# Performance work log

Hardware: AMD Instinct MI355X
Metric: run time of the kernel (lower is better)

Reference implementation:

```python
import jax, jax.numpy as jnp
import numpy as np

HIDDEN = 1024
HEADS = 16
HEAD_DIM = HIDDEN // HEADS


def setup_inputs() -> dict:
    key = jax.random.key(0)
    ks = jax.random.split(key, 9)
    B, S = 2, 2048
    std = 1.0 / np.sqrt(HIDDEN)
    inp = {
        'hidden_states': jax.random.normal(ks[0], (B, S, HIDDEN), dtype=jnp.float32),
        'attention_mask': jnp.ones((B, S), dtype=jnp.int32),
        'wq': jax.random.normal(ks[1], (HIDDEN, HIDDEN), dtype=jnp.float32) * std,
        'bq': jnp.zeros((HIDDEN,), dtype=jnp.float32),
        'wk': jax.random.normal(ks[2], (HIDDEN, HIDDEN), dtype=jnp.float32) * std,
        'bk': jnp.zeros((HIDDEN,), dtype=jnp.float32),
        'wv': jax.random.normal(ks[3], (HIDDEN, HIDDEN), dtype=jnp.float32) * std,
        'bv': jnp.zeros((HIDDEN,), dtype=jnp.float32),
        'wo': jax.random.normal(ks[4], (HIDDEN, HIDDEN), dtype=jnp.float32) * std,
        'bo': jnp.zeros((HIDDEN,), dtype=jnp.float32),
    }
    return inp


def reference(hidden_states, attention_mask, wq, bq, wk, bk, wv, bv, wo, bo):
    B, S, H = hidden_states.shape
    def heads(x):  # [B,S,H] -> [B,nh,S,hd]
        return x.reshape(B, S, HEADS, HEAD_DIM).transpose(0, 2, 1, 3)
    q = heads(hidden_states @ wq + bq)
    k = heads(hidden_states @ wk + bk)
    v = heads(hidden_states @ wv + bv)
    scores = jnp.einsum('bhqd,bhkd->bhqk', q, k) / np.sqrt(HEAD_DIM).astype(np.float32)
    causal = jnp.tril(jnp.ones((S, S), dtype=bool))  # True = keep
    keep = causal[None, None] & (attention_mask[:, None, None, :] != 0)
    scores = jnp.where(keep, scores, -jnp.inf)
    probs = jax.nn.softmax(scores, axis=-1)
    out = jnp.einsum('bhqk,bhkd->bhqd', probs, v)  # [B,nh,S,hd]
    out = out.transpose(0, 2, 1, 3).reshape(B, S, H)
    return out @ wo + bo
```

## Files before the change

kernel.cpp:

```cpp
#include <hip/hip_runtime.h>

#define HID   1024
#define SLEN  2048
#define NHEAD 16
#define HDIM  64
#define SC2L  0.18033688f

typedef unsigned short u16;
typedef _Float16 f16;
using bf16x8 = __attribute__((ext_vector_type(8))) short;
using f16x4  = __attribute__((ext_vector_type(4))) f16;
using f32x4  = __attribute__((ext_vector_type(4))) float;

typedef __attribute__((address_space(1))) void gvoid;
typedef __attribute__((address_space(3))) void lvoid;

__device__ __forceinline__ u16 f2bf(float f) {
  union { float f; unsigned u; } v; v.f = f;
  unsigned u = v.u;
  return (u16)((u + 0x7fffu + ((u >> 16) & 1u)) >> 16);
}

__device__ __forceinline__ void async_ld16(const u16* g, u16* l) {
  __builtin_amdgcn_global_load_lds((gvoid*)g, (lvoid*)l, 16, 0, 0);
}

__global__ __launch_bounds__(256) void prep_kernel(const float* __restrict__ x,
                                                   const float* __restrict__ wq,
                                                   const float* __restrict__ wk,
                                                   const float* __restrict__ wv,
                                                   const float* __restrict__ wo,
                                                   u16* __restrict__ xb,
                                                   u16* __restrict__ wt) {
  const int tid = threadIdx.x;
  if (blockIdx.z == 4) {
    const int bid = blockIdx.y * 32 + blockIdx.x;
#pragma unroll
    for (int it = 0; it < 4; ++it) {
      const int i = bid * 1024 + it * 256 + tid;
      float4 v = ((const float4*)x)[i];
      ushort4 o;
      o.x = f2bf(v.x); o.y = f2bf(v.y); o.z = f2bf(v.z); o.w = f2bf(v.w);
      ((ushort4*)xb)[i] = o;
    }
    return;
  }
  const float* src = (blockIdx.z == 0) ? wq : (blockIdx.z == 1) ? wk
                   : (blockIdx.z == 2) ? wv : wo;
  u16* dst = wt + (size_t)blockIdx.z * (HID * HID);
  __shared__ float tile[32][33];
  const int n0 = blockIdx.x * 32, k0 = blockIdx.y * 32;
  const int xx = tid & 31, yy = tid >> 5;
  for (int i = yy; i < 32; i += 8)
    tile[i][xx] = src[(size_t)(k0 + i) * HID + n0 + xx];
  __syncthreads();
  for (int i = yy; i < 32; i += 8)
    dst[(size_t)(n0 + i) * HID + k0 + xx] = f2bf(tile[xx][i]);
}

__global__ __launch_bounds__(256) void gemm_qkv_kernel(const u16* __restrict__ A,
                                                       const u16* __restrict__ Bt,
                                                       const float* __restrict__ bq,
                                                       const float* __restrict__ bk,
                                                       const float* __restrict__ bv,
                                                       u16* __restrict__ Qb,
                                                       u16* __restrict__ Kb,
                                                       u16* __restrict__ VTf) {
  __shared__ u16 smem[8192];
  u16* sA = smem;
  u16* sB = smem + 4096;
  const int tid  = threadIdx.x;
  const int wave = tid >> 6, lane = tid & 63;
  const int quad = lane >> 4, l16 = lane & 15;
  const int n0g = blockIdx.x * 128;
  const int region = blockIdx.x >> 3;
  const int colbase = (blockIdx.x & 7) * 128;
  const int m0 = blockIdx.y * 128;
  const int wm = (wave & 1) * 64, wn = (wave >> 1) * 64;

  f32x4 acc[4][4] = {};
  const int srow = lane >> 2;
  const int scol = (lane & 3) * 8;

  for (int kt = 0; kt < HID; kt += 32) {
    __syncthreads();
    for (int c = wave; c < 8; c += 4) {
      async_ld16(A  + (size_t)(m0  + c * 16 + srow) * HID + kt + scol, &sA[c * 512]);
      async_ld16(Bt + (size_t)(n0g + c * 16 + srow) * HID + kt + scol, &sB[c * 512]);
    }
    __syncthreads();

    bf16x8 af[4], bfr[4];
#pragma unroll
    for (int t = 0; t < 4; ++t) {
      af[t]  = *(const bf16x8*)&sA[(wm + t * 16 + l16) * 32 + quad * 8];
      bfr[t] = *(const bf16x8*)&sB[(wn + t * 16 + l16) * 32 + quad * 8];
    }
#pragma unroll
    for (int mt = 0; mt < 4; ++mt)
#pragma unroll
      for (int nt = 0; nt < 4; ++nt)
        acc[mt][nt] = __builtin_amdgcn_mfma_f32_16x16x32_bf16(af[mt], bfr[nt],
                                                              acc[mt][nt], 0, 0, 0);
  }

  const float* bias = (region == 0) ? bq : (region == 1) ? bk : bv;
  float bvv[4];
#pragma unroll
  for (int nt = 0; nt < 4; ++nt) bvv[nt] = bias[colbase + wn + nt * 16 + l16];

  if (region == 2) {
    const int bb = m0 >> 11;
    const int m0loc = m0 & 2047;
    const int h0 = colbase >> 6;
    u16* T = smem;
#pragma unroll
    for (int h2 = 0; h2 < 2; ++h2) {
      __syncthreads();
      if ((wave >> 1) == h2) {
#pragma unroll
        for (int mt = 0; mt < 4; ++mt)
#pragma unroll
          for (int nt = 0; nt < 4; ++nt)
#pragma unroll
            for (int r = 0; r < 4; ++r) {
              const int sl = (wave & 1) * 64 + mt * 16 + quad * 4 + r;
              const int dl = nt * 16 + l16;
              union { f16 h; u16 u; } cv;
              cv.h = (f16)(acc[mt][nt][r] + bvv[nt]);
              T[dl * 128 + (((sl >> 3) ^ l16) * 8) + (sl & 7)] = cv.u;
            }
      }
      __syncthreads();
      const int d = tid >> 2, sg = (tid & 3) * 4;
      u16* slab0 = VTf + ((size_t)((bb * NHEAD + h0 + h2) * 128 + (m0loc >> 4))) * 1024;
#pragma unroll
      for (int cc = 0; cc < 4; ++cc) {
        const int cl = sg + cc;
        const int ph = cl ^ (d & 15);
        const int slot = (d * 2 + (cl & 1)) ^ ((d >> 2) & 1);
        *(bf16x8*)(slab0 + (size_t)(cl >> 1) * 1024 + slot * 8)
            = *(const bf16x8*)&T[d * 128 + ph * 8];
      }
    }
    return;
  }

  u16* C = (region == 0) ? Qb : Kb;
#pragma unroll
  for (int mt = 0; mt < 4; ++mt)
#pragma unroll
    for (int r = 0; r < 4; ++r) {
      const int row = m0 + wm + mt * 16 + quad * 4 + r;
#pragma unroll
      for (int nt = 0; nt < 4; ++nt) {
        const int col = colbase + wn + nt * 16 + l16;
        C[(size_t)row * HID + col] = f2bf(acc[mt][nt][r] + bvv[nt]);
      }
    }
}

__global__ __launch_bounds__(256) void gemm_o_kernel(const u16* __restrict__ A,
                                                     const u16* __restrict__ Bt,
                                                     const float* __restrict__ bias,
                                                     float* __restrict__ Cf) {
  __shared__ u16 sA[64 * 32];
  __shared__ u16 sB[128 * 32];
  const int tid  = threadIdx.x;
  const int wave = tid >> 6, lane = tid & 63;
  const int quad = lane >> 4, l16 = lane & 15;
  const int n0 = blockIdx.x * 128;
  const int m0 = blockIdx.y * 64;
  const int wn = wave * 32;

  f32x4 acc[4][2] = {};
  const int srow = lane >> 2;
  const int scol = (lane & 3) * 8;

  for (int kt = 0; kt < HID; kt += 32) {
    __syncthreads();
    for (int c = wave; c < 12; c += 4) {
      if (c < 4) async_ld16(A  + (size_t)(m0 + c * 16 + srow) * HID + kt + scol, &sA[c * 512]);
      else       async_ld16(Bt + (size_t)(n0 + (c - 4) * 16 + srow) * HID + kt + scol,
                            &sB[(c - 4) * 512]);
    }
    __syncthreads();

    bf16x8 af[4], bfr[2];
#pragma unroll
    for (int t = 0; t < 4; ++t)
      af[t] = *(const bf16x8*)&sA[(t * 16 + l16) * 32 + quad * 8];
#pragma unroll
    for (int t = 0; t < 2; ++t)
      bfr[t] = *(const bf16x8*)&sB[(wn + t * 16 + l16) * 32 + quad * 8];
#pragma unroll
    for (int mt = 0; mt < 4; ++mt)
#pragma unroll
      for (int nt = 0; nt < 2; ++nt)
        acc[mt][nt] = __builtin_amdgcn_mfma_f32_16x16x32_bf16(af[mt], bfr[nt],
                                                              acc[mt][nt], 0, 0, 0);
  }

  float bvv[2];
#pragma unroll
  for (int nt = 0; nt < 2; ++nt) bvv[nt] = bias[n0 + wn + nt * 16 + l16];
#pragma unroll
  for (int mt = 0; mt < 4; ++mt)
#pragma unroll
    for (int r = 0; r < 4; ++r) {
      const int row = m0 + mt * 16 + quad * 4 + r;
#pragma unroll
      for (int nt = 0; nt < 2; ++nt)
        Cf[(size_t)row * HID + n0 + wn + nt * 16 + l16] = acc[mt][nt][r] + bvv[nt];
    }
}

__global__ __launch_bounds__(256, 2) void flash_attn_kernel(const u16* __restrict__ Q,
                                                            const u16* __restrict__ K,
                                                            const u16* __restrict__ VT,
                                                            const int* __restrict__ mask,
                                                            u16* __restrict__ O) {
  const int xb = blockIdx.x, h = blockIdx.y, b = blockIdx.z;
  const int tid  = threadIdx.x;
  const int wave = tid >> 6, lane = tid & 63;
  const int quad = lane >> 4, l16 = lane & 15;

  __shared__ alignas(16) char smraw[35840];
  u16*   Ks  = (u16*)smraw;
  u16*   Vt  = (u16*)(smraw + 16384);
  float* Ob0 = (float*)smraw;
  float* Ob1 = (float*)(smraw + 16896);
  float* lb  = (float*)(smraw + 33792);

  const u16* Kh  = K  + (size_t)b * SLEN * HID + h * HDIM;
  const u16* Vth = VT + (size_t)(b * NHEAD + h) * (128 * 1024);

  const int srow8 = lane >> 3;
  const int gch   = (lane & 7) ^ srow8;
  const int rx    = l16 & 7;

  for (int phase = 0; phase < 2; ++phase) {
    const int qt = phase ? (31 - xb) : xb;
    const int q0 = qt * 64;

    bf16x8 qb[4][2];
#pragma unroll
    for (int nt = 0; nt < 4; ++nt) {
      const u16* qp = Q + (size_t)(b * SLEN + q0 + nt * 16 + l16) * HID + h * HDIM + quad * 8;
      qb[nt][0] = *(const bf16x8*)qp;
      qb[nt][1] = *(const bf16x8*)(qp + 32);
    }

    f32x4 oacc[4][4] = {};
    float l_part[4] = {0.f, 0.f, 0.f, 0.f};

    {
      const int r0 = wave * 16 + srow8;
      u16* kd = Ks + wave * 1024;
      async_ld16(Kh + (size_t)r0 * HID + gch * 8,       kd);
      async_ld16(Kh + (size_t)(r0 + 8) * HID + gch * 8, kd + 512);
      const u16* vs = Vth + (size_t)wave * 1024;
      u16* vd = Vt + wave * 1024;
      async_ld16(vs + lane * 8,        vd);
      async_ld16(vs + (64 + lane) * 8, vd + 512);
    }
    int4 mi = *(const int4*)(mask + b * SLEN + wave * 16 + quad * 4);

    for (int j = 0; j <= qt; ++j) {
      const int buf = j & 1;
      u16* KsB = Ks + buf * 4096;
      u16* VtB = Vt + buf * 4096;

      int4 mi_n = mi;
      if (j < qt) {
        const int nb = (buf ^ 1) * 4096;
        const int jn = j + 1;
        const int r0 = wave * 16 + srow8;
        u16* kd = Ks + nb + wave * 1024;
        async_ld16(Kh + (size_t)(jn * 64 + r0) * HID + gch * 8,     kd);
        async_ld16(Kh + (size_t)(jn * 64 + r0 + 8) * HID + gch * 8, kd + 512);
        const u16* vs = Vth + (size_t)(jn * 4 + wave) * 1024;
        u16* vd = Vt + nb + wave * 1024;
        async_ld16(vs + lane * 8,        vd);
        async_ld16(vs + (64 + lane) * 8, vd + 512);
        asm volatile("s_waitcnt vmcnt(4)" ::: "memory");
        mi_n = *(const int4*)(mask + b * SLEN + jn * 64 + wave * 16 + quad * 4);
      } else {
        asm volatile("s_waitcnt vmcnt(0)" ::: "memory");
      }

      float map[4];
      map[0] = mi.x ? 0.f : -1e30f;  map[1] = mi.y ? 0.f : -1e30f;
      map[2] = mi.z ? 0.f : -1e30f;  map[3] = mi.w ? 0.f : -1e30f;

      const u16* kp = KsB + (wave * 16 + l16) * 64;
      const int ph0 = quad ^ rx;
      const bf16x8 ka0 = *(const bf16x8*)(kp + ph0 * 8);
      const bf16x8 ka1 = *(const bf16x8*)(kp + (ph0 ^ 4) * 8);

      float p[4][4];
#pragma unroll
      for (int nt = 0; nt < 4; ++nt) {
        f32x4 z = {0.f, 0.f, 0.f, 0.f};
        z = __builtin_amdgcn_mfma_f32_16x16x32_bf16(ka0, qb[nt][0], z, 0, 0, 0);
        z = __builtin_amdgcn_mfma_f32_16x16x32_bf16(ka1, qb[nt][1], z, 0, 0, 0);
#pragma unroll
        for (int r = 0; r < 4; ++r)
          p[nt][r] = exp2f(fmaf(z[r], SC2L, map[r]));
      }
      if (j == qt) {
#pragma unroll
        for (int nt = 0; nt < 4; ++nt)
#pragma unroll
          for (int r = 0; r < 4; ++r)
            if (wave * 16 + quad * 4 + r > nt * 16 + l16) p[nt][r] = 0.f;
      }

      f16x4 pb[4];
#pragma unroll
      for (int nt = 0; nt < 4; ++nt) {
        l_part[nt] += (p[nt][0] + p[nt][1]) + (p[nt][2] + p[nt][3]);
        pb[nt][0] = (f16)p[nt][0]; pb[nt][1] = (f16)p[nt][1];
        pb[nt][2] = (f16)p[nt][2]; pb[nt][3] = (f16)p[nt][3];
      }

#pragma unroll
      for (int dt = 0; dt < 4; ++dt) {
        const int dd = dt * 16 + l16;
        const int slot = (dd * 2 + (quad >> 1)) ^ ((dd >> 2) & 1);
        const f16x4 va = *(const f16x4*)(VtB + wave * 1024 + slot * 8 + (quad & 1) * 4);
#pragma unroll
        for (int nt = 0; nt < 4; ++nt)
          oacc[dt][nt] = __builtin_amdgcn_mfma_f32_16x16x16f16(va, pb[nt], oacc[dt][nt], 0, 0, 0);
      }
      mi = mi_n;
    }

    __syncthreads();

#pragma unroll
    for (int nt = 0; nt < 4; ++nt) {
      l_part[nt] += __shfl_xor(l_part[nt], 16);
      l_part[nt] += __shfl_xor(l_part[nt], 32);
    }
    if (quad == 0)
#pragma unroll
      for (int nt = 0; nt < 4; ++nt) lb[wave * 64 + nt * 16 + l16] = l_part[nt];

    if ((wave & 1) == 0) {
      float* ob = (wave == 0) ? Ob0 : Ob1;
#pragma unroll
      for (int dt = 0; dt < 4; ++dt)
#pragma unroll
        for (int nt = 0; nt < 4; ++nt)
#pragma unroll
          for (int r = 0; r < 4; ++r)
            ob[(dt * 16 + quad * 4 + r) * 66 + nt * 16 + l16] = oacc[dt][nt][r];
    }
    __syncthreads();
    if (wave & 1) {
      float* ob = (wave == 1) ? Ob0 : Ob1;
#pragma unroll
      for (int dt = 0; dt < 4; ++dt)
#pragma unroll
        for (int nt = 0; nt < 4; ++nt)
#pragma unroll
          for (int r = 0; r < 4; ++r)
            ob[(dt * 16 + quad * 4 + r) * 66 + nt * 16 + l16] += oacc[dt][nt][r];
    }
    __syncthreads();

    {
      const int q  = tid >> 2;
      const int dc = tid & 3;
      const float l = lb[q] + lb[64 + q] + lb[128 + q] + lb[192 + q];
      const float inv = 1.f / l;
      u16 ob[16];
#pragma unroll
      for (int e = 0; e < 16; ++e) {
        const int d = dc * 16 + e;
        ob[e] = f2bf((Ob0[d * 66 + q] + Ob1[d * 66 + q]) * inv);
      }
      u16* op = O + (size_t)(b * SLEN + q0 + q) * HID + h * HDIM + dc * 16;
      *(bf16x8*)op       = *(bf16x8*)&ob[0];
      *(bf16x8*)(op + 8) = *(bf16x8*)&ob[8];
    }
    __syncthreads();
  }
}

extern "C" void kernel_launch(void* const* d_in, const int* in_sizes, int n_in,
                              void* d_out, int out_size, void* d_ws, size_t ws_size,
                              hipStream_t stream) {
  const float* x    = (const float*)d_in[0];
  const int*   mask = (const int*)d_in[1];
  const float* wq   = (const float*)d_in[2];
  const float* bq   = (const float*)d_in[3];
  const float* wk   = (const float*)d_in[4];
  const float* bk   = (const float*)d_in[5];
  const float* wv   = (const float*)d_in[6];
  const float* bv   = (const float*)d_in[7];
  const float* wo   = (const float*)d_in[8];
  const float* bo   = (const float*)d_in[9];
  float* out = (float*)d_out;

  char* ws = (char*)d_ws;
  u16* XBF = (u16*)(ws);
  u16* WT  = (u16*)(ws + (8u  << 20));
  u16* QBF = (u16*)(ws + (16u << 20));
  u16* KBF = (u16*)(ws + (24u << 20));
  u16* VTF = (u16*)(ws + (32u << 20));
  u16* ATT = (u16*)(ws);

  prep_kernel<<<dim3(32, 32, 5), 256, 0, stream>>>(x, wq, wk, wv, wo, XBF, WT);
  gemm_qkv_kernel<<<dim3(24, 32), 256, 0, stream>>>(XBF, WT, bq, bk, bv, QBF, KBF, VTF);
  flash_attn_kernel<<<dim3(16, NHEAD, 2), 256, 0, stream>>>(QBF, KBF, VTF, mask, ATT);
  gemm_o_kernel<<<dim3(8, 64), 256, 0, stream>>>(ATT, WT + (3u << 20), bo, out);
}
```

Measured before the change: 199.2 us.

## Triple-buffer K/V tiles, precompute mask bits, use packed f16 conversion

Extends the K/V staging in flash attention from double to triple buffering, prefetching two tiles ahead with adjusted waitcnt thresholds to hide more global load latency. The per-tile mask loads are replaced by a one-time bitmask held in registers and read with a lane shuffle. Probability conversion to f16 now uses packed round-toward-zero conversions. Shared memory per block grows, and the RTZ rounding slightly changes numerics.

```diff
diff --git a/kernel.cpp b/kernel.cpp
--- a/kernel.cpp
+++ b/kernel.cpp
@@ -9,6 +9,7 @@
 typedef unsigned short u16;
 typedef _Float16 f16;
 using bf16x8 = __attribute__((ext_vector_type(8))) short;
+using h16x2  = __attribute__((ext_vector_type(2))) __fp16;
 using f16x4  = __attribute__((ext_vector_type(4))) f16;
 using f32x4  = __attribute__((ext_vector_type(4))) float;
 
@@ -225,9 +226,9 @@
   const int wave = tid >> 6, lane = tid & 63;
   const int quad = lane >> 4, l16 = lane & 15;
 
-  __shared__ alignas(16) char smraw[35840];
+  __shared__ alignas(16) char smraw[49152];
   u16*   Ks  = (u16*)smraw;
-  u16*   Vt  = (u16*)(smraw + 16384);
+  u16*   Vt  = (u16*)(smraw + 24576);
   float* Ob0 = (float*)smraw;
   float* Ob1 = (float*)(smraw + 16896);
   float* lb  = (float*)(smraw + 33792);
@@ -238,6 +239,20 @@
   const int srow8 = lane >> 3;
   const int gch   = (lane & 7) ^ srow8;
   const int rx    = l16 & 7;
+
+  unsigned mw = 0;
+  {
+    const int4* mrow = (const int4*)(mask + b * SLEN);
+#pragma unroll
+    for (int c = 0; c < 8; ++c) {
+      int4 m = mrow[lane * 8 + c];
+      mw |= (m.x ? 1u : 0u) << (c * 4);
+      mw |= (m.y ? 1u : 0u) << (c * 4 + 1);
+      mw |= (m.z ? 1u : 0u) << (c * 4 + 2);
+      mw |= (m.w ? 1u : 0u) << (c * 4 + 3);
+    }
+  }
+  const int mb = (wave & 1) * 16 + quad * 4;
 
   for (int phase = 0; phase < 2; ++phase) {
     const int qt = phase ? (31 - xb) : xb;
@@ -254,44 +269,41 @@
     f32x4 oacc[4][4] = {};
     float l_part[4] = {0.f, 0.f, 0.f, 0.f};
 
-    {
-      const int r0 = wave * 16 + srow8;
-      u16* kd = Ks + wave * 1024;
-      async_ld16(Kh + (size_t)r0 * HID + gch * 8,       kd);
-      async_ld16(Kh + (size_t)(r0 + 8) * HID + gch * 8, kd + 512);
-      const u16* vs = Vth + (size_t)wave * 1024;
-      u16* vd = Vt + wave * 1024;
-      async_ld16(vs + lane * 8,        vd);
-      async_ld16(vs + (64 + lane) * 8, vd + 512);
-    }
-    int4 mi = *(const int4*)(mask + b * SLEN + wave * 16 + quad * 4);
-
+    const int r0s = wave * 16 + srow8;
+#define STAGE_KV(jt, bufi)                                                      \
+    {                                                                           \
+      u16* kd = Ks + (bufi) * 4096 + wave * 1024;                               \
+      async_ld16(Kh + (size_t)((jt) * 64 + r0s) * HID + gch * 8,       kd);     \
+      async_ld16(Kh + (size_t)((jt) * 64 + r0s + 8) * HID + gch * 8,   kd + 512);\
+      const u16* vs = Vth + (size_t)((jt) * 4 + wave) * 1024;                   \
+      u16* vd = Vt + (bufi) * 4096 + wave * 1024;                               \
+      async_ld16(vs + lane * 8,        vd);                                     \
+      async_ld16(vs + (64 + lane) * 8, vd + 512);                               \
+    }
+
+    STAGE_KV(0, 0);
+    if (qt >= 1) STAGE_KV(1, 1);
+
+    int cur = 0;
     for (int j = 0; j <= qt; ++j) {
-      const int buf = j & 1;
-      u16* KsB = Ks + buf * 4096;
-      u16* VtB = Vt + buf * 4096;
-
-      int4 mi_n = mi;
-      if (j < qt) {
-        const int nb = (buf ^ 1) * 4096;
-        const int jn = j + 1;
-        const int r0 = wave * 16 + srow8;
-        u16* kd = Ks + nb + wave * 1024;
-        async_ld16(Kh + (size_t)(jn * 64 + r0) * HID + gch * 8,     kd);
-        async_ld16(Kh + (size_t)(jn * 64 + r0 + 8) * HID + gch * 8, kd + 512);
-        const u16* vs = Vth + (size_t)(jn * 4 + wave) * 1024;
-        u16* vd = Vt + nb + wave * 1024;
-        async_ld16(vs + lane * 8,        vd);
-        async_ld16(vs + (64 + lane) * 8, vd + 512);
+      u16* KsB = Ks + cur * 4096;
+      u16* VtB = Vt + cur * 4096;
+
+      if (j + 2 <= qt) {
+        const int b2 = (cur == 0) ? 2 : cur - 1;
+        STAGE_KV(j + 2, b2);
+        asm volatile("s_waitcnt vmcnt(8)" ::: "memory");
+      } else if (j + 1 <= qt) {
         asm volatile("s_waitcnt vmcnt(4)" ::: "memory");
-        mi_n = *(const int4*)(mask + b * SLEN + jn * 64 + wave * 16 + quad * 4);
       } else {
         asm volatile("s_waitcnt vmcnt(0)" ::: "memory");
       }
 
+      const unsigned wbits = __shfl(mw, 2 * j + (wave >> 1));
       float map[4];
-      map[0] = mi.x ? 0.f : -1e30f;  map[1] = mi.y ? 0.f : -1e30f;
-      map[2] = mi.z ? 0.f : -1e30f;  map[3] = mi.w ? 0.f : -1e30f;
+#pragma unroll
+      for (int r = 0; r < 4; ++r)
+        map[r] = ((wbits >> (mb + r)) & 1u) ? 0.f : -1e30f;
 
       const u16* kp = KsB + (wave * 16 + l16) * 64;
       const int ph0 = quad ^ rx;
@@ -320,8 +332,10 @@
 #pragma unroll
       for (int nt = 0; nt < 4; ++nt) {
         l_part[nt] += (p[nt][0] + p[nt][1]) + (p[nt][2] + p[nt][3]);
-        pb[nt][0] = (f16)p[nt][0]; pb[nt][1] = (f16)p[nt][1];
-        pb[nt][2] = (f16)p[nt][2]; pb[nt][3] = (f16)p[nt][3];
+        union { h16x2 h[2]; f16x4 v; } u;
+        u.h[0] = __builtin_amdgcn_cvt_pkrtz(p[nt][0], p[nt][1]);
+        u.h[1] = __builtin_amdgcn_cvt_pkrtz(p[nt][2], p[nt][3]);
+        pb[nt] = u.v;
       }
 
 #pragma unroll
@@ -333,8 +347,9 @@
         for (int nt = 0; nt < 4; ++nt)
           oacc[dt][nt] = __builtin_amdgcn_mfma_f32_16x16x16f16(va, pb[nt], oacc[dt][nt], 0, 0, 0);
       }
-      mi = mi_n;
-    }
+      cur = (cur == 2) ? 0 : cur + 1;
+    }
+#undef STAGE_KV
 
     __syncthreads();
 
```

Measured after the change: 203.5 us. +2.2%, slower.

## Double-buffer GEMM LDS loads, remap block order, enlarge O-proj tiles

Applied to the files above, without the earlier changes.

Both GEMM kernels now double-buffer their LDS tiles, issuing async global-to-LDS loads for the next K step while MFMAs run on the current one. Ordering is enforced with explicit vmcnt waits and raw barriers. Block indices are remapped so that consecutive blocks are spread across the grid, likely to improve L2 locality or XCD distribution. The output projection moves from 64x128 to 128x128 tiles with 4x4 MFMA accumulators per wave, halving the block count and adding register pressure and LDS use.

```diff
diff --git a/kernel.cpp b/kernel.cpp
--- a/kernel.cpp
+++ b/kernel.cpp
@@ -66,30 +66,44 @@
                                                        u16* __restrict__ Qb,
                                                        u16* __restrict__ Kb,
                                                        u16* __restrict__ VTf) {
-  __shared__ u16 smem[8192];
-  u16* sA = smem;
-  u16* sB = smem + 4096;
+  __shared__ u16 smem[16384];
   const int tid  = threadIdx.x;
   const int wave = tid >> 6, lane = tid & 63;
   const int quad = lane >> 4, l16 = lane & 15;
-  const int n0g = blockIdx.x * 128;
-  const int region = blockIdx.x >> 3;
-  const int colbase = (blockIdx.x & 7) * 128;
-  const int m0 = blockIdx.y * 128;
+  const int raw = blockIdx.y * 24 + blockIdx.x;
+  const int logi = (raw & 7) * 96 + (raw >> 3);
+  const int bx = logi % 24, by = logi / 24;
+  const int n0g = bx * 128;
+  const int region = bx >> 3;
+  const int colbase = (bx & 7) * 128;
+  const int m0 = by * 128;
   const int wm = (wave & 1) * 64, wn = (wave >> 1) * 64;
 
   f32x4 acc[4][4] = {};
   const int srow = lane >> 2;
   const int scol = (lane & 3) * 8;
 
-  for (int kt = 0; kt < HID; kt += 32) {
-    __syncthreads();
-    for (int c = wave; c < 8; c += 4) {
-      async_ld16(A  + (size_t)(m0  + c * 16 + srow) * HID + kt + scol, &sA[c * 512]);
-      async_ld16(Bt + (size_t)(n0g + c * 16 + srow) * HID + kt + scol, &sB[c * 512]);
-    }
-    __syncthreads();
-
+#define STAGE_G(kt, bi)                                                          \
+  for (int c = wave; c < 8; c += 4) {                                            \
+    async_ld16(A  + (size_t)(m0  + c * 16 + srow) * HID + (kt) + scol,           \
+               &smem[(bi) * 8192 + c * 512]);                                    \
+    async_ld16(Bt + (size_t)(n0g + c * 16 + srow) * HID + (kt) + scol,           \
+               &smem[(bi) * 8192 + 4096 + c * 512]);                             \
+  }
+
+  STAGE_G(0, 0);
+  for (int ks = 0; ks < 32; ++ks) {
+    const int bi = ks & 1;
+    if (ks < 31) {
+      STAGE_G((ks + 1) * 32, bi ^ 1);
+      asm volatile("s_waitcnt vmcnt(4)" ::: "memory");
+    } else {
+      asm volatile("s_waitcnt vmcnt(0)" ::: "memory");
+    }
+    __builtin_amdgcn_s_barrier();
+
+    const u16* sA = smem + bi * 8192;
+    const u16* sB = smem + bi * 8192 + 4096;
     bf16x8 af[4], bfr[4];
 #pragma unroll
     for (int t = 0; t < 4; ++t) {
@@ -102,7 +116,9 @@
       for (int nt = 0; nt < 4; ++nt)
         acc[mt][nt] = __builtin_amdgcn_mfma_f32_16x16x32_bf16(af[mt], bfr[nt],
                                                               acc[mt][nt], 0, 0, 0);
-  }
+    __builtin_amdgcn_s_barrier();
+  }
+#undef STAGE_G
 
   const float* bias = (region == 0) ? bq : (region == 1) ? bk : bv;
   float bvv[4];
@@ -164,53 +180,67 @@
                                                      const u16* __restrict__ Bt,
                                                      const float* __restrict__ bias,
                                                      float* __restrict__ Cf) {
-  __shared__ u16 sA[64 * 32];
-  __shared__ u16 sB[128 * 32];
+  __shared__ u16 smem[16384];
   const int tid  = threadIdx.x;
   const int wave = tid >> 6, lane = tid & 63;
   const int quad = lane >> 4, l16 = lane & 15;
-  const int n0 = blockIdx.x * 128;
-  const int m0 = blockIdx.y * 64;
-  const int wn = wave * 32;
-
-  f32x4 acc[4][2] = {};
+  const int raw = blockIdx.x;
+  const int logi = (raw & 7) * 32 + (raw >> 3);
+  const int n0 = (logi & 7) * 128;
+  const int m0 = (logi >> 3) * 128;
+  const int wm = (wave & 1) * 64, wn = (wave >> 1) * 64;
+
+  f32x4 acc[4][4] = {};
   const int srow = lane >> 2;
   const int scol = (lane & 3) * 8;
 
-  for (int kt = 0; kt < HID; kt += 32) {
-    __syncthreads();
-    for (int c = wave; c < 12; c += 4) {
-      if (c < 4) async_ld16(A  + (size_t)(m0 + c * 16 + srow) * HID + kt + scol, &sA[c * 512]);
-      else       async_ld16(Bt + (size_t)(n0 + (c - 4) * 16 + srow) * HID + kt + scol,
-                            &sB[(c - 4) * 512]);
-    }
-    __syncthreads();
-
-    bf16x8 af[4], bfr[2];
-#pragma unroll
-    for (int t = 0; t < 4; ++t)
-      af[t] = *(const bf16x8*)&sA[(t * 16 + l16) * 32 + quad * 8];
-#pragma unroll
-    for (int t = 0; t < 2; ++t)
+#define STAGE_O(kt, bi)                                                          \
+  for (int c = wave; c < 8; c += 4) {                                            \
+    async_ld16(A  + (size_t)(m0 + c * 16 + srow) * HID + (kt) + scol,            \
+               &smem[(bi) * 8192 + c * 512]);                                    \
+    async_ld16(Bt + (size_t)(n0 + c * 16 + srow) * HID + (kt) + scol,            \
+               &smem[(bi) * 8192 + 4096 + c * 512]);                             \
+  }
+
+  STAGE_O(0, 0);
+  for (int ks = 0; ks < 32; ++ks) {
+    const int bi = ks & 1;
+    if (ks < 31) {
+      STAGE_O((ks + 1) * 32, bi ^ 1);
+      asm volatile("s_waitcnt vmcnt(4)" ::: "memory");
+    } else {
+      asm volatile("s_waitcnt vmcnt(0)" ::: "memory");
+    }
+    __builtin_amdgcn_s_barrier();
+
+    const u16* sA = smem + bi * 8192;
+    const u16* sB = smem + bi * 8192 + 4096;
+    bf16x8 af[4], bfr[4];
+#pragma unroll
+    for (int t = 0; t < 4; ++t) {
+      af[t]  = *(const bf16x8*)&sA[(wm + t * 16 + l16) * 32 + quad * 8];
       bfr[t] = *(const bf16x8*)&sB[(wn + t * 16 + l16) * 32 + quad * 8];
+    }
 #pragma unroll
     for (int mt = 0; mt < 4; ++mt)
 #pragma unroll
-      for (int nt = 0; nt < 2; ++nt)
+      for (int nt = 0; nt < 4; ++nt)
         acc[mt][nt] = __builtin_amdgcn_mfma_f32_16x16x32_bf16(af[mt], bfr[nt],
                                                               acc[mt][nt], 0, 0, 0);
-  }
-
-  float bvv[2];
-#pragma unroll
-  for (int nt = 0; nt < 2; ++nt) bvv[nt] = bias[n0 + wn + nt * 16 + l16];
+    __builtin_amdgcn_s_barrier();
+  }
+#undef STAGE_O
+
+  float bvv[4];
+#pragma unroll
+  for (int nt = 0; nt < 4; ++nt) bvv[nt] = bias[n0 + wn + nt * 16 + l16];
 #pragma unroll
   for (int mt = 0; mt < 4; ++mt)
 #pragma unroll
     for (int r = 0; r < 4; ++r) {
-      const int row = m0 + mt * 16 + quad * 4 + r;
-#pragma unroll
-      for (int nt = 0; nt < 2; ++nt)
+      const int row = m0 + wm + mt * 16 + quad * 4 + r;
+#pragma unroll
+      for (int nt = 0; nt < 4; ++nt)
         Cf[(size_t)row * HID + n0 + wn + nt * 16 + l16] = acc[mt][nt][r] + bvv[nt];
     }
 }
@@ -415,5 +445,5 @@
   prep_kernel<<<dim3(32, 32, 5), 256, 0, stream>>>(x, wq, wk, wv, wo, XBF, WT);
   gemm_qkv_kernel<<<dim3(24, 32), 256, 0, stream>>>(XBF, WT, bq, bk, bv, QBF, KBF, VTF);
   flash_attn_kernel<<<dim3(16, NHEAD, 2), 256, 0, stream>>>(QBF, KBF, VTF, mask, ATT);
-  gemm_o_kernel<<<dim3(8, 64), 256, 0, stream>>>(ATT, WT + (3u << 20), bo, out);
-}
+  gemm_o_kernel<<<dim3(256), 256, 0, stream>>>(ATT, WT + (3u << 20), bo, out);
+}
```

New measurement: 196.2 us. Within noise of the previous version (-1.5%).

## Double-buffer async LDS loads in both GEMMs and enlarge QKV tiles

Applied to the files above, without the earlier changes.

Both projection GEMMs now double-buffer their shared-memory tiles so the global-to-LDS loads for the next K-step are issued before computing the current one, using manual vmcnt waits and raw barriers. The QKV GEMM grows to 256x256 tiles with 512 threads (8x4 MFMA tiles per wave) and a 1D grid remapped so that consecutive blocks are spread across XCDs; the O GEMM gets a similar block remap. The V-transpose epilogue is adapted to the wider tile. This targets load latency and the two full barriers per K-step, at the cost of more LDS (64 KB) and registers, and a QKV grid of only 192 blocks.

```diff
diff --git a/kernel.cpp b/kernel.cpp
--- a/kernel.cpp
+++ b/kernel.cpp
@@ -58,7 +58,7 @@
     dst[(size_t)(n0 + i) * HID + k0 + xx] = f2bf(tile[xx][i]);
 }
 
-__global__ __launch_bounds__(256) void gemm_qkv_kernel(const u16* __restrict__ A,
+__global__ __launch_bounds__(512) void gemm_qkv_kernel(const u16* __restrict__ A,
                                                        const u16* __restrict__ Bt,
                                                        const float* __restrict__ bq,
                                                        const float* __restrict__ bk,
@@ -66,43 +66,63 @@
                                                        u16* __restrict__ Qb,
                                                        u16* __restrict__ Kb,
                                                        u16* __restrict__ VTf) {
-  __shared__ u16 smem[8192];
-  u16* sA = smem;
-  u16* sB = smem + 4096;
+  __shared__ u16 smem[32768];
   const int tid  = threadIdx.x;
   const int wave = tid >> 6, lane = tid & 63;
   const int quad = lane >> 4, l16 = lane & 15;
-  const int n0g = blockIdx.x * 128;
-  const int region = blockIdx.x >> 3;
-  const int colbase = (blockIdx.x & 7) * 128;
-  const int m0 = blockIdx.y * 128;
-  const int wm = (wave & 1) * 64, wn = (wave >> 1) * 64;
-
-  f32x4 acc[4][4] = {};
+  const int raw = blockIdx.x;
+  const int logi = (raw & 7) * 24 + (raw >> 3);
+  const int bxn = logi % 12;
+  const int by  = logi / 12;
+  const int n0g = bxn * 256;
+  const int region = bxn >> 2;
+  const int colbase = (bxn & 3) * 256;
+  const int m0 = by * 256;
+  const int wm = (wave & 1) * 128, wn = (wave >> 1) * 64;
+
+  f32x4 acc[8][4] = {};
   const int srow = lane >> 2;
   const int scol = (lane & 3) * 8;
 
-  for (int kt = 0; kt < HID; kt += 32) {
-    __syncthreads();
-    for (int c = wave; c < 8; c += 4) {
-      async_ld16(A  + (size_t)(m0  + c * 16 + srow) * HID + kt + scol, &sA[c * 512]);
-      async_ld16(Bt + (size_t)(n0g + c * 16 + srow) * HID + kt + scol, &sB[c * 512]);
-    }
-    __syncthreads();
-
-    bf16x8 af[4], bfr[4];
-#pragma unroll
-    for (int t = 0; t < 4; ++t) {
+#define STAGE_G(kt, bi)                                                          \
+  for (int c = wave; c < 32; c += 8) {                                           \
+    if (c < 16)                                                                  \
+      async_ld16(A  + (size_t)(m0  + c * 16 + srow) * HID + (kt) + scol,         \
+                 &smem[(bi) * 16384 + c * 512]);                                 \
+    else                                                                         \
+      async_ld16(Bt + (size_t)(n0g + (c - 16) * 16 + srow) * HID + (kt) + scol,  \
+                 &smem[(bi) * 16384 + 8192 + (c - 16) * 512]);                   \
+  }
+
+  STAGE_G(0, 0);
+  for (int ks = 0; ks < 32; ++ks) {
+    const int bi = ks & 1;
+    if (ks < 31) {
+      STAGE_G((ks + 1) * 32, bi ^ 1);
+      asm volatile("s_waitcnt vmcnt(4)" ::: "memory");
+    } else {
+      asm volatile("s_waitcnt vmcnt(0)" ::: "memory");
+    }
+    __builtin_amdgcn_s_barrier();
+
+    const u16* sA = smem + bi * 16384;
+    const u16* sB = smem + bi * 16384 + 8192;
+    bf16x8 af[8], bfr[4];
+#pragma unroll
+    for (int t = 0; t < 8; ++t)
       af[t]  = *(const bf16x8*)&sA[(wm + t * 16 + l16) * 32 + quad * 8];
+#pragma unroll
+    for (int t = 0; t < 4; ++t)
       bfr[t] = *(const bf16x8*)&sB[(wn + t * 16 + l16) * 32 + quad * 8];
-    }
-#pragma unroll
-    for (int mt = 0; mt < 4; ++mt)
+#pragma unroll
+    for (int mt = 0; mt < 8; ++mt)
 #pragma unroll
       for (int nt = 0; nt < 4; ++nt)
         acc[mt][nt] = __builtin_amdgcn_mfma_f32_16x16x32_bf16(af[mt], bfr[nt],
                                                               acc[mt][nt], 0, 0, 0);
-  }
+    __builtin_amdgcn_s_barrier();
+  }
+#undef STAGE_G
 
   const float* bias = (region == 0) ? bq : (region == 1) ? bk : bv;
   float bvv[4];
@@ -115,32 +135,32 @@
     const int h0 = colbase >> 6;
     u16* T = smem;
 #pragma unroll
-    for (int h2 = 0; h2 < 2; ++h2) {
+    for (int h2 = 0; h2 < 4; ++h2) {
       __syncthreads();
       if ((wave >> 1) == h2) {
 #pragma unroll
-        for (int mt = 0; mt < 4; ++mt)
+        for (int mt = 0; mt < 8; ++mt)
 #pragma unroll
           for (int nt = 0; nt < 4; ++nt)
 #pragma unroll
             for (int r = 0; r < 4; ++r) {
-              const int sl = (wave & 1) * 64 + mt * 16 + quad * 4 + r;
+              const int sl = wm + mt * 16 + quad * 4 + r;
               const int dl = nt * 16 + l16;
               union { f16 h; u16 u; } cv;
               cv.h = (f16)(acc[mt][nt][r] + bvv[nt]);
-              T[dl * 128 + (((sl >> 3) ^ l16) * 8) + (sl & 7)] = cv.u;
+              T[dl * 256 + (((sl >> 3) ^ (dl & 31)) * 8) + (sl & 7)] = cv.u;
             }
       }
       __syncthreads();
-      const int d = tid >> 2, sg = (tid & 3) * 4;
+      const int d = tid >> 3, sg = (tid & 7) * 4;
       u16* slab0 = VTf + ((size_t)((bb * NHEAD + h0 + h2) * 128 + (m0loc >> 4))) * 1024;
 #pragma unroll
       for (int cc = 0; cc < 4; ++cc) {
         const int cl = sg + cc;
-        const int ph = cl ^ (d & 15);
+        const int ph = cl ^ (d & 31);
         const int slot = (d * 2 + (cl & 1)) ^ ((d >> 2) & 1);
         *(bf16x8*)(slab0 + (size_t)(cl >> 1) * 1024 + slot * 8)
-            = *(const bf16x8*)&T[d * 128 + ph * 8];
+            = *(const bf16x8*)&T[d * 256 + ph * 8];
       }
     }
     return;
@@ -148,7 +168,7 @@
 
   u16* C = (region == 0) ? Qb : Kb;
 #pragma unroll
-  for (int mt = 0; mt < 4; ++mt)
+  for (int mt = 0; mt < 8; ++mt)
 #pragma unroll
     for (int r = 0; r < 4; ++r) {
       const int row = m0 + wm + mt * 16 + quad * 4 + r;
@@ -164,28 +184,41 @@
                                                      const u16* __restrict__ Bt,
                                                      const float* __restrict__ bias,
                                                      float* __restrict__ Cf) {
-  __shared__ u16 sA[64 * 32];
-  __shared__ u16 sB[128 * 32];
+  __shared__ u16 smem[12288];
   const int tid  = threadIdx.x;
   const int wave = tid >> 6, lane = tid & 63;
   const int quad = lane >> 4, l16 = lane & 15;
-  const int n0 = blockIdx.x * 128;
-  const int m0 = blockIdx.y * 64;
+  const int raw = blockIdx.y * 8 + blockIdx.x;
+  const int logi = (raw & 7) * 64 + (raw >> 3);
+  const int n0 = (logi & 7) * 128;
+  const int m0 = (logi >> 3) * 64;
   const int wn = wave * 32;
 
   f32x4 acc[4][2] = {};
   const int srow = lane >> 2;
   const int scol = (lane & 3) * 8;
 
-  for (int kt = 0; kt < HID; kt += 32) {
-    __syncthreads();
-    for (int c = wave; c < 12; c += 4) {
-      if (c < 4) async_ld16(A  + (size_t)(m0 + c * 16 + srow) * HID + kt + scol, &sA[c * 512]);
-      else       async_ld16(Bt + (size_t)(n0 + (c - 4) * 16 + srow) * HID + kt + scol,
-                            &sB[(c - 4) * 512]);
-    }
-    __syncthreads();
-
+#define STAGE_O(kt, bi)                                                          \
+  for (int c = wave; c < 12; c += 4) {                                           \
+    if (c < 4) async_ld16(A + (size_t)(m0 + c * 16 + srow) * HID + (kt) + scol,  \
+                          &smem[(bi) * 6144 + c * 512]);                         \
+    else async_ld16(Bt + (size_t)(n0 + (c - 4) * 16 + srow) * HID + (kt) + scol, \
+                    &smem[(bi) * 6144 + 2048 + (c - 4) * 512]);                  \
+  }
+
+  STAGE_O(0, 0);
+  for (int ks = 0; ks < 32; ++ks) {
+    const int bi = ks & 1;
+    if (ks < 31) {
+      STAGE_O((ks + 1) * 32, bi ^ 1);
+      asm volatile("s_waitcnt vmcnt(3)" ::: "memory");
+    } else {
+      asm volatile("s_waitcnt vmcnt(0)" ::: "memory");
+    }
+    __builtin_amdgcn_s_barrier();
+
+    const u16* sA = smem + bi * 6144;
+    const u16* sB = smem + bi * 6144 + 2048;
     bf16x8 af[4], bfr[2];
 #pragma unroll
     for (int t = 0; t < 4; ++t)
@@ -199,7 +232,9 @@
       for (int nt = 0; nt < 2; ++nt)
         acc[mt][nt] = __builtin_amdgcn_mfma_f32_16x16x32_bf16(af[mt], bfr[nt],
                                                               acc[mt][nt], 0, 0, 0);
-  }
+    __builtin_amdgcn_s_barrier();
+  }
+#undef STAGE_O
 
   float bvv[2];
 #pragma unroll
@@ -413,7 +448,7 @@
   u16* ATT = (u16*)(ws);
 
   prep_kernel<<<dim3(32, 32, 5), 256, 0, stream>>>(x, wq, wk, wv, wo, XBF, WT);
-  gemm_qkv_kernel<<<dim3(24, 32), 256, 0, stream>>>(XBF, WT, bq, bk, bv, QBF, KBF, VTF);
+  gemm_qkv_kernel<<<dim3(192), 512, 0, stream>>>(XBF, WT, bq, bk, bv, QBF, KBF, VTF);
   flash_attn_kernel<<<dim3(16, NHEAD, 2), 256, 0, stream>>>(QBF, KBF, VTF, mask, ATT);
   gemm_o_kernel<<<dim3(8, 64), 256, 0, stream>>>(ATT, WT + (3u << 20), bo, out);
 }
```

Result: slower. 205.6 us (+3.2%).
